# Performance work log

Measured on AMD Instinct MI355X. Metric: run time of the kernel, lower is better.

## Reference

```python
import jax, jax.numpy as jnp
import numpy as np

TAU = 2.0        # MultiStepLIFNode tau
ALPHA = 4.0      # sigmoid surrogate-gradient sharpness (spikingjelly default)
BN_EPS = 1e-5

@jax.custom_vjp
def heaviside(x):
    return (x >= 0.0).astype(x.dtype)

def _h_fwd(x):
    return (x >= 0.0).astype(x.dtype), x

def _h_bwd(res, g):
    s = jax.nn.sigmoid(ALPHA * res)
    return (g * ALPHA * s * (1.0 - s),)

heaviside.defvjp(_h_fwd, _h_bwd)

def lif(x_seq, v_threshold=1.0):
    """Multi-step LIF, hard reset to 0, decay_input, detach_reset. x_seq: [T, ...]"""
    def step(v, x):
        v = v + (x - v) / TAU
        spike = heaviside(v - v_threshold)
        v = v * (1.0 - jax.lax.stop_gradient(spike))
        return v, spike
    _, spikes = jax.lax.scan(step, jnp.zeros_like(x_seq[0]), x_seq)
    return spikes

def conv1x1_bn(x, w, gamma, beta, mean, var, bias=None):
    # x: [T,B,C,H,W]; 1x1 conv == channel matmul; BN in eval mode (affine fold)
    y = jnp.einsum('tbchw,oc->tbohw', x, w)
    if bias is not None:
        y = y + bias[None, None, :, None, None]
    inv = gamma / jnp.sqrt(var + BN_EPS)
    return y * inv[None, None, :, None, None] + (beta - mean * inv)[None, None, :, None, None]

def setup_inputs() -> dict:
    key = jax.random.key(0)
    T, B, C, H, W = 4, 16, 512, 32, 32
    ks = jax.random.split(key, 18)
    def w(k):
        return jax.random.normal(k, (C, C), jnp.float32) * (1.0 / np.sqrt(C))
    def vec_n(k):
        return jax.random.normal(k, (C,), jnp.float32) * 0.1
    def vec_p(k):
        return jax.random.uniform(k, (C,), jnp.float32, 0.5, 1.5)
    return {
        'x': jax.random.normal(ks[0], (T, B, C, H, W), jnp.float32),
        'q_w': w(ks[1]), 'q_gamma': vec_p(ks[2]), 'q_beta': vec_n(ks[3]),
        'q_mean': vec_n(ks[4]), 'q_var': vec_p(ks[5]),
        'k_w': w(ks[6]), 'k_gamma': vec_p(ks[7]), 'k_beta': vec_n(ks[8]),
        'k_mean': vec_n(ks[9]), 'k_var': vec_p(ks[10]),
        'proj_w': w(ks[11]), 'proj_b': vec_n(ks[12]), 'proj_gamma': vec_p(ks[13]),
        'proj_beta': vec_n(ks[14]), 'proj_mean': vec_n(ks[15]), 'proj_var': vec_p(ks[16]),
        'num_heads': 8,
    }

def reference(x, q_w, q_gamma, q_beta, q_mean, q_var,
              k_w, k_gamma, k_beta, k_mean, k_var,
              proj_w, proj_b, proj_gamma, proj_beta, proj_mean, proj_var,
              num_heads):
    T, B, C, H, W = x.shape
    hd = C // num_heads
    # Q / K branches: conv1x1 -> BN -> LIF spikes
    q = lif(conv1x1_bn(x, q_w, q_gamma, q_beta, q_mean, q_var))          # [T,B,C,H,W]
    k = lif(conv1x1_bn(x, k_w, k_gamma, k_beta, k_mean, k_var))          # [T,B,C,H,W]
    # sum over head-channel dim (keepdim), spike-gate at threshold 0.5
    q = q.reshape(T, B, num_heads, hd, H, W).sum(axis=3, keepdims=True)  # [T,B,nh,1,H,W]
    attn = lif(q, v_threshold=0.5)                                       # [T,B,nh,1,H,W]
    # elementwise gated attention (broadcast over head channels)
    y = (attn * k.reshape(T, B, num_heads, hd, H, W)).reshape(T, B, C, H, W)
    # projection: conv1x1(+bias) -> BN -> LIF
    y = lif(conv1x1_bn(y, proj_w, proj_gamma, proj_beta, proj_mean, proj_var, bias=proj_b))
    return y
```

## Files before the change

### kernel.cpp

```cpp
#include <hip/hip_runtime.h>
#include <cstdint>
#include <math.h>

#define TT 4
#define BB 16
#define CCH 512
#define HWD 1024
#define NHH 8
#define NW 16
#define MQK 1.5e-4
#define MPROJ 1.0e-4
#define CAPQ 49152
#define CAPP 16384
#define WTSZ 262144

typedef __attribute__((ext_vector_type(4))) float f32x4;
typedef __attribute__((ext_vector_type(8))) short s16x8;
typedef __attribute__((ext_vector_type(4))) uint32_t u32x4;

static __device__ __forceinline__ f32x4 MFMA(s16x8 a, s16x8 b, f32x4 c) {
    return __builtin_amdgcn_mfma_f32_16x16x32_bf16(a, b, c, 0, 0, 0);
}

static __device__ __forceinline__ uint32_t hi_pair(uint32_t u0, uint32_t u1) {
#if __has_builtin(__builtin_amdgcn_perm)
    return __builtin_amdgcn_perm(u1, u0, 0x07060302u);
#else
    return (u1 & 0xFFFF0000u) | (u0 >> 16);
#endif
}

struct SplitPair { uint32_t h, l; };

static __device__ __forceinline__ SplitPair split_pair(float f0, float f1) {
    const uint32_t u0 = __builtin_bit_cast(uint32_t, f0);
    const uint32_t u1 = __builtin_bit_cast(uint32_t, f1);
    SplitPair r;
    r.h = hi_pair(u0, u1);
    const float r0 = f0 - __builtin_bit_cast(float, u0 & 0xFFFF0000u);
    const float r1 = f1 - __builtin_bit_cast(float, u1 & 0xFFFF0000u);
    r.l = hi_pair(__builtin_bit_cast(uint32_t, r0), __builtin_bit_cast(uint32_t, r1));
    return r;
}

static __device__ __forceinline__ void load_split_frag(const float* p, s16x8& h, s16x8& l) {
    const float4 a = *(const float4*)p;
    const float4 b4 = *(const float4*)(p + 4);
    u32x4 hw_, lw_;
    const SplitPair p0 = split_pair(a.x, a.y);
    const SplitPair p1 = split_pair(a.z, a.w);
    const SplitPair p2 = split_pair(b4.x, b4.y);
    const SplitPair p3 = split_pair(b4.z, b4.w);
    hw_[0] = p0.h; lw_[0] = p0.l;
    hw_[1] = p1.h; lw_[1] = p1.l;
    hw_[2] = p2.h; lw_[2] = p2.l;
    hw_[3] = p3.h; lw_[3] = p3.l;
    h = __builtin_bit_cast(s16x8, hw_);
    l = __builtin_bit_cast(s16x8, lw_);
}

static __device__ __forceinline__ void glds16(const float* g, float* l) {
    __builtin_amdgcn_global_load_lds(
        (const __attribute__((address_space(1))) uint32_t*)g,
        (__attribute__((address_space(3))) uint32_t*)l, 16, 0, 0);
}

static __device__ __forceinline__ void probe_bf16(int lane, int rowD[4], int colD[4],
                                                  int& aRow, int& aKb, int& bCol, int& bKb)
{
    const f32x4 z = {0.f, 0.f, 0.f, 0.f};
    const short lv = (short)(__builtin_bit_cast(uint32_t, (float)lane) >> 16);
    const short one = (short)0x3F80;
    const s16x8 av = {lv, lv, lv, lv, lv, lv, lv, lv};
    const s16x8 ov = {one, one, one, one, one, one, one, one};
    const f32x4 pa = MFMA(av, ov, z);
    const f32x4 pb = MFMA(ov, av, z);
    bool A2 = false, B2 = false;
#pragma unroll
    for (int r = 0; r < 4; ++r) {
        const int va = (int)pa[r];
        if (((va - 48) & 127) == 0) { rowD[r] = (va - 48) >> 7; A2 = true; }
        else                        { rowD[r] = (va - 768) >> 5; }
        const int vb = (int)pb[r];
        if (((vb - 48) & 127) == 0) { colD[r] = (vb - 48) >> 7; B2 = true; }
        else                        { colD[r] = (vb - 768) >> 5; }
    }
    aRow = A2 ? (lane >> 2) : (lane & 15);
    aKb  = A2 ? (lane & 3) * 8 : (lane >> 4) * 8;
    bCol = B2 ? (lane >> 2) : (lane & 15);
    bKb  = B2 ? (lane & 3) * 8 : (lane >> 4) * 8;
}

__global__ void k_zero(unsigned int* ctr) {
    if (threadIdx.x < 2) ctr[threadIdx.x] = 0u;
}

__global__ __launch_bounds__(256) void k_prep(
    const float* __restrict__ qw, const float* __restrict__ kw, const float* __restrict__ pw,
    const float* __restrict__ qg, const float* __restrict__ qbe,
    const float* __restrict__ qm, const float* __restrict__ qva,
    const float* __restrict__ kg, const float* __restrict__ kbe,
    const float* __restrict__ km, const float* __restrict__ kva,
    const float* __restrict__ pg, const float* __restrict__ pbe,
    const float* __restrict__ pm, const float* __restrict__ pva,
    const float* __restrict__ pb,
    unsigned short* __restrict__ wt, double* __restrict__ bnc)
{
    const int bx = blockIdx.x;
    const int mat = bx >> 5, ot = bx & 31;
    const float* W = (mat == 0) ? qw : ((mat == 1) ? kw : pw);
    unsigned short* hi = wt + (size_t)(mat * 2 + 0) * WTSZ;
    unsigned short* lo = wt + (size_t)(mat * 2 + 1) * WTSZ;
#pragma unroll
    for (int it = 0; it < 4; ++it) {
        const int j = it * 256 + threadIdx.x;
        const int ks = j >> 6, sub = j & 63;
        const int kgrp = sub >> 4, row = sub & 15;
        const float* src = W + (size_t)(ot * 16 + row) * CCH + ks * 32 + kgrp * 8;
        s16x8 h, l;
        load_split_frag(src, h, l);
        *(s16x8*)&hi[((size_t)(ot * 16 + ks) * 64 + sub) * 8] = h;
        *(s16x8*)&lo[((size_t)(ot * 16 + ks) * 64 + sub) * 8] = l;
    }
    if (ot == 0) {
        const float* g  = (mat == 0) ? qg  : ((mat == 1) ? kg  : pg);
        const float* be = (mat == 0) ? qbe : ((mat == 1) ? kbe : pbe);
        const float* mn = (mat == 0) ? qm  : ((mat == 1) ? km  : pm);
        const float* va = (mat == 0) ? qva : ((mat == 1) ? kva : pva);
        for (int o = threadIdx.x; o < CCH; o += 256) {
            const double inv = (double)g[o] / sqrt((double)va[o] + 1e-5);
            double add = (double)be[o] - (double)mn[o] * inv;
            if (mat == 2) add = add + (double)pb[o] * inv;
            bnc[(size_t)(mat * CCH + o) * 2]     = inv;
            bnc[(size_t)(mat * CCH + o) * 2 + 1] = add;
        }
    }
}

__global__ __launch_bounds__(256, 4) void k_qk(
    const float* __restrict__ x,
    const unsigned short* __restrict__ wt, const double* __restrict__ bnc,
    uint32_t* __restrict__ qbits, uint32_t* __restrict__ kbits,
    unsigned int* __restrict__ ctr, uint32_t* __restrict__ list)
{
    __shared__ float Xs[2][4096];
    __shared__ uint32_t QB[2][2][TT][32];

    const int tid = threadIdx.x, lane = tid & 63, wid = tid >> 6;
    const int b   = blockIdx.z;
    const int o0  = blockIdx.y * 64, hw0 = blockIdx.x * 32;
    const int worow = (wid >> 1) * 32, whw = (wid & 1) * 16;

    int rowD[4], colD[4], aRow, aKb, bCol, bKb;
    probe_bf16(lane, rowD, colD, aRow, aKb, bCol, bKb);

    const int laneoff = ((aKb >> 3) * 16 + aRow) * 8;
    const int kgrp = bKb >> 3;
    const int roff = (whw + bCol) ^ ((kgrp & 1) << 4);
    const int otg0 = blockIdx.y * 4 + (wid >> 1) * 2;

    uint32_t gOff[4];
#pragma unroll
    for (int it = 0; it < 4; ++it) {
        const int ch = it * 256 + tid;
        const int t = ch >> 8, c = (ch >> 3) & 31, hw4p = ch & 7;
        const int ghw4 = hw4p ^ (((c >> 3) & 1) << 2);
        gOff[it] = (uint32_t)(((t * BB + b) * CCH + c) * HWD + hw0 + ghw4 * 4);
    }

    f32x4 aq[TT][2], ak[TT][2];
#pragma unroll
    for (int t = 0; t < TT; ++t)
#pragma unroll
        for (int ot = 0; ot < 2; ++ot) {
            aq[t][ot] = (f32x4){0.f, 0.f, 0.f, 0.f};
            ak[t][ot] = (f32x4){0.f, 0.f, 0.f, 0.f};
        }

    auto stage = [&](int ks, int buf) {
#pragma unroll
        for (int it = 0; it < 4; ++it)
            glds16(x + (size_t)gOff[it] + (size_t)ks * (32 * HWD),
                   &Xs[buf][(it * 256 + wid * 64) * 4]);
    };

    stage(0, 0);

    int cur = 0;
#pragma unroll 1
    for (int ks = 0; ks < 16; ++ks) {
        __syncthreads();
        if (ks < 15) stage(ks + 1, cur ^ 1);

        const size_t tb0 = ((size_t)(otg0 + 0) * 16 + ks) * 512 + laneoff;
        const size_t tb1 = ((size_t)(otg0 + 1) * 16 + ks) * 512 + laneoff;
        const s16x8 Aqh0 = *(const s16x8*)&wt[0 * WTSZ + tb0];
        const s16x8 Aql0 = *(const s16x8*)&wt[1 * WTSZ + tb0];
        const s16x8 Akh0 = *(const s16x8*)&wt[2 * WTSZ + tb0];
        const s16x8 Akl0 = *(const s16x8*)&wt[3 * WTSZ + tb0];
        const s16x8 Aqh1 = *(const s16x8*)&wt[0 * WTSZ + tb1];
        const s16x8 Aql1 = *(const s16x8*)&wt[1 * WTSZ + tb1];
        const s16x8 Akh1 = *(const s16x8*)&wt[2 * WTSZ + tb1];
        const s16x8 Akl1 = *(const s16x8*)&wt[3 * WTSZ + tb1];

        const float* Bb = Xs[cur];
#pragma unroll
        for (int t = 0; t < TT; ++t) {
            const float* Bp = Bb + (t * 32 + kgrp * 8) * 32 + roff;
            float w[8];
#pragma unroll
            for (int e = 0; e < 8; ++e) w[e] = Bp[e * 32];
            u32x4 bh, bl;
#pragma unroll
            for (int p = 0; p < 4; ++p) {
                const SplitPair sp = split_pair(w[2 * p], w[2 * p + 1]);
                bh[p] = sp.h; bl[p] = sp.l;
            }
            const s16x8 Bh = __builtin_bit_cast(s16x8, bh);
            const s16x8 Bl = __builtin_bit_cast(s16x8, bl);

            aq[t][0] = MFMA(Aqh0, Bh, aq[t][0]);
            aq[t][0] = MFMA(Aqh0, Bl, aq[t][0]);
            aq[t][0] = MFMA(Aql0, Bh, aq[t][0]);
            ak[t][0] = MFMA(Akh0, Bh, ak[t][0]);
            ak[t][0] = MFMA(Akh0, Bl, ak[t][0]);
            ak[t][0] = MFMA(Akl0, Bh, ak[t][0]);
            aq[t][1] = MFMA(Aqh1, Bh, aq[t][1]);
            aq[t][1] = MFMA(Aqh1, Bl, aq[t][1]);
            aq[t][1] = MFMA(Aql1, Bh, aq[t][1]);
            ak[t][1] = MFMA(Akh1, Bh, ak[t][1]);
            ak[t][1] = MFMA(Akh1, Bl, ak[t][1]);
            ak[t][1] = MFMA(Akl1, Bh, ak[t][1]);
        }
        cur ^= 1;
    }

    {
        int dum0, dum1, dum2, dum3;
        probe_bf16(lane, rowD, colD, dum0, dum1, dum2, dum3);
    }
    ((uint32_t*)QB)[tid] = 0u;
    ((uint32_t*)QB)[tid + 256] = 0u;
    __syncthreads();

    auto chains = [&](f32x4 (&acc)[TT][2], int br) {
#pragma unroll
        for (int ot = 0; ot < 2; ++ot)
#pragma unroll
            for (int r = 0; r < 4; ++r) {
                const int orow = worow + ot * 16 + rowD[r];
                const int o = o0 + orow;
                const double inv = bnc[(size_t)(br * CCH + o) * 2];
                const double add = bnc[(size_t)(br * CCH + o) * 2 + 1];
                const uint32_t bit = 1u << (orow & 31);
                const int ow = orow >> 5;
                const int hwq = whw + colD[r];
                double v = 0.0; bool fl = false;
#pragma unroll
                for (int t = 0; t < TT; ++t) {
                    const double y = (double)acc[t][ot][r] * inv + add;
                    v = v + (y - v) * 0.5;
                    if (fabs(v - 1.0) < MQK) fl = true;
                    if (v >= 1.0) { atomicOr(&QB[br][ow][t][hwq], bit); v = 0.0; }
                }
                if (fl) {
                    const unsigned int idx = atomicAdd(ctr, 1u);
                    if (idx < CAPQ)
                        list[idx] = (uint32_t)((br << 23) | (o << 14) | (b << 10) | (hw0 + hwq));
                }
            }
    };
    chains(aq, 0);
    chains(ak, 1);
    __syncthreads();

#pragma unroll
    for (int u = 0; u < 2; ++u) {
        const int idx = tid + u * 256;
        const int br = idx >> 8, ow = (idx >> 7) & 1, t = (idx >> 5) & 3, hwq = idx & 31;
        uint32_t* dst = br ? kbits : qbits;
        dst[((size_t)(t * BB + b) * NW + (o0 >> 5) + ow) * HWD + hw0 + hwq] = QB[br][ow][t][hwq];
    }
}

__global__ __launch_bounds__(256) void k_fix_qk(
    const float* __restrict__ x,
    const float* __restrict__ qw, const float* __restrict__ qg, const float* __restrict__ qbe,
    const float* __restrict__ qm, const float* __restrict__ qva,
    const float* __restrict__ kw, const float* __restrict__ kg, const float* __restrict__ kbe,
    const float* __restrict__ km, const float* __restrict__ kva,
    const unsigned int* __restrict__ ctr, const uint32_t* __restrict__ list,
    uint32_t* __restrict__ qbits, uint32_t* __restrict__ kbits)
{
    const int lane = threadIdx.x & 63;
    const int wg = (blockIdx.x * blockDim.x + threadIdx.x) >> 6;
    const int nw = (gridDim.x * blockDim.x) >> 6;
    unsigned int n = *ctr; if (n > CAPQ) n = CAPQ;

    for (unsigned int i = wg; i < n; i += nw) {
        const uint32_t e = list[i];
        const int br = (e >> 23) & 1, o = (e >> 14) & 511, b = (e >> 10) & 15, hw = e & 1023;
        const float* w = (br ? kw : qw) + (size_t)o * CCH;
        double dots[TT];
#pragma unroll
        for (int t = 0; t < TT; ++t) {
            double s = 0.0;
            for (int c = lane; c < CCH; c += 64)
                s += (double)w[c] * (double)x[((size_t)(t * BB + b) * CCH + c) * HWD + hw];
#pragma unroll
            for (int off = 32; off; off >>= 1) s += __shfl_xor(s, off);
            dots[t] = s;
        }
        if (lane == 0) {
            const float* g  = br ? kg  : qg;
            const float* be = br ? kbe : qbe;
            const float* mn = br ? km  : qm;
            const float* va = br ? kva : qva;
            const double inv = (double)g[o] / sqrt((double)va[o] + 1e-5);
            const double add = (double)be[o] - (double)mn[o] * inv;
            uint32_t* bits = br ? kbits : qbits;
            double v = 0.0;
#pragma unroll
            for (int t = 0; t < TT; ++t) {
                const double y = dots[t] * inv + add;
                v = v + (y - v) * 0.5;
                const size_t wa = ((size_t)(t * BB + b) * NW + (o >> 5)) * HWD + hw;
                const uint32_t bit = 1u << (o & 31);
                if (v >= 1.0) { atomicOr(&bits[wa], bit); v = 0.0; }
                else          { atomicAnd(&bits[wa], ~bit); }
            }
        }
    }
}

__global__ __launch_bounds__(256) void k_attn(
    const uint32_t* __restrict__ qbits, uint8_t* __restrict__ attn)
{
    const int idx = blockIdx.x * 256 + threadIdx.x;
    const int hw = idx & (HWD - 1);
    const int h  = (idx >> 10) & (NHH - 1);
    const int b  = idx >> 13;
    double v = 0.0;
#pragma unroll
    for (int t = 0; t < TT; ++t) {
        const uint32_t w0 = qbits[((size_t)(t * BB + b) * NW + h * 2    ) * HWD + hw];
        const uint32_t w1 = qbits[((size_t)(t * BB + b) * NW + h * 2 + 1) * HWD + hw];
        const double q = (double)(__popc(w0) + __popc(w1));
        v = v + (q - v) * 0.5;
        const uint8_t s = (v >= 0.5) ? (uint8_t)1 : (uint8_t)0;
        attn[((size_t)(t * BB + b) * NHH + h) * HWD + hw] = s;
        if (s) v = 0.0;
    }
}

__global__ __launch_bounds__(256, 3) void k_proj(
    const unsigned short* __restrict__ wt, const double* __restrict__ bnc,
    const uint32_t* __restrict__ kbits, const uint8_t* __restrict__ attn,
    float* __restrict__ out,
    unsigned int* __restrict__ ctr2, uint32_t* __restrict__ list2)
{
    __shared__ __align__(16) unsigned short Aw[2][2][8][512];

    const int tid = threadIdx.x, lane = tid & 63, wid = tid >> 6;
    const int b   = blockIdx.z;
    const int o0  = blockIdx.y * 128, hw0 = blockIdx.x * 32;
    const int worow = (wid >> 1) * 64, whw = (wid & 1) * 16;

    int rowD[4], colD[4], aRow, aKb, bCol, bKb;
    probe_bf16(lane, rowD, colD, aRow, aKb, bCol, bKb);
    const int laneoff = ((aKb >> 3) * 16 + aRow) * 8;
    const int hwB = hw0 + whw + bCol;
    const int otl0 = (wid >> 1) * 4;

    f32x4 acc[TT][4];
#pragma unroll
    for (int t = 0; t < TT; ++t)
#pragma unroll
        for (int ot = 0; ot < 4; ++ot) acc[t][ot] = (f32x4){0.f, 0.f, 0.f, 0.f};

    auto stageA = [&](int ks, int buf) {
#pragma unroll
        for (int i = 0; i < 4; ++i) {
            const int ch = wid * 4 + i;
            const int plane = ch >> 3, otl = ch & 7;
            const unsigned short* src = wt + (size_t)(4 + plane) * WTSZ
                + ((size_t)(blockIdx.y * 8 + otl) * 16 + ks) * 512 + (size_t)lane * 8;
            glds16((const float*)src, (float*)&Aw[buf][plane][otl][0]);
        }
    };

    uint32_t kvc[TT], avc[TT], kvn[TT], avn[TT];
    auto loadB = [&](int ks, uint32_t kv[TT], uint32_t av[TT]) {
#pragma unroll
        for (int t = 0; t < TT; ++t) {
            const size_t tb = (size_t)(t * BB + b);
            kv[t] = kbits[(tb * NW + ks) * HWD + hwB];
            av[t] = attn[(tb * NHH + (ks >> 1)) * HWD + hwB];
        }
    };

    stageA(0, 0);
    loadB(0, kvc, avc);
    __syncthreads();

    int cur = 0;
#pragma unroll 1
    for (int ks = 0; ks < 16; ++ks) {
        if (ks < 15) { stageA(ks + 1, cur ^ 1); loadB(ks + 1, kvn, avn); }

        s16x8 Ah[4], Al[4];
#pragma unroll
        for (int ot = 0; ot < 4; ++ot) {
            Ah[ot] = *(const s16x8*)&Aw[cur][0][otl0 + ot][laneoff];
            Al[ot] = *(const s16x8*)&Aw[cur][1][otl0 + ot][laneoff];
        }
#pragma unroll
        for (int t = 0; t < TT; ++t) {
            const uint32_t mask = avc[t] ? kvc[t] : 0u;
            const uint32_t byt = (mask >> bKb) & 0xFFu;
            u32x4 bw;
#pragma unroll
            for (int j = 0; j < 4; ++j)
                bw[j] = (((byt >> (2 * j)) & 1u) ? 0x3F80u : 0u)
                      | (((byt >> (2 * j + 1)) & 1u) ? 0x3F800000u : 0u);
            const s16x8 By = __builtin_bit_cast(s16x8, bw);
#pragma unroll
            for (int ot = 0; ot < 4; ++ot) {
                acc[t][ot] = MFMA(Ah[ot], By, acc[t][ot]);
                acc[t][ot] = MFMA(Al[ot], By, acc[t][ot]);
            }
        }

        if (ks < 15) {
#pragma unroll
            for (int t = 0; t < TT; ++t) { kvc[t] = kvn[t]; avc[t] = avn[t]; }
        }
        __syncthreads();
        cur ^= 1;
    }

#pragma unroll
    for (int ot = 0; ot < 4; ++ot)
#pragma unroll
        for (int r = 0; r < 4; ++r) {
            const int o = o0 + worow + ot * 16 + rowD[r];
            const int hwD = hw0 + whw + colD[r];
            const double inv = bnc[(size_t)(2 * CCH + o) * 2];
            const double add = bnc[(size_t)(2 * CCH + o) * 2 + 1];
            double v = 0.0; bool fl = false;
#pragma unroll
            for (int t = 0; t < TT; ++t) {
                const double y = (double)acc[t][ot][r] * inv + add;
                v = v + (y - v) * 0.5;
                if (fabs(v - 1.0) < MPROJ) fl = true;
                float s;
                if (v >= 1.0) { s = 1.0f; v = 0.0; } else { s = 0.0f; }
                out[((size_t)(t * BB + b) * CCH + o) * HWD + hwD] = s;
            }
            if (fl) {
                const unsigned int idx = atomicAdd(ctr2, 1u);
                if (idx < CAPP) list2[idx] = (uint32_t)((o << 14) | (b << 10) | hwD);
            }
        }
}

__global__ __launch_bounds__(256) void k_fix_proj(
    const float* __restrict__ pw, const float* __restrict__ pb,
    const float* __restrict__ pg, const float* __restrict__ pbe,
    const float* __restrict__ pm, const float* __restrict__ pva,
    const uint32_t* __restrict__ kbits, const uint8_t* __restrict__ attn,
    const unsigned int* __restrict__ ctr2, const uint32_t* __restrict__ list2,
    float* __restrict__ out)
{
    const int lane = threadIdx.x & 63;
    const int wg = (blockIdx.x * blockDim.x + threadIdx.x) >> 6;
    const int nw = (gridDim.x * blockDim.x) >> 6;
    unsigned int n = *ctr2; if (n > CAPP) n = CAPP;

    for (unsigned int i = wg; i < n; i += nw) {
        const uint32_t e = list2[i];
        const int o = (e >> 14) & 511, b = (e >> 10) & 15, hw = e & 1023;
        const float* w = pw + (size_t)o * CCH;
        double dots[TT];
#pragma unroll
        for (int t = 0; t < TT; ++t) {
            double s = 0.0;
            for (int c = lane; c < CCH; c += 64) {
                const uint32_t kv = kbits[((size_t)(t * BB + b) * NW + (c >> 5)) * HWD + hw];
                const uint32_t av = attn[((size_t)(t * BB + b) * NHH + (c >> 6)) * HWD + hw];
                if (av && ((kv >> (c & 31)) & 1u)) s += (double)w[c];
            }
#pragma unroll
            for (int off = 32; off; off >>= 1) s += __shfl_xor(s, off);
            dots[t] = s;
        }
        if (lane == 0) {
            const double inv = (double)pg[o] / sqrt((double)pva[o] + 1e-5);
            const double add = (double)pbe[o] - (double)pm[o] * inv;
            const double bias = (double)pb[o];
            double v = 0.0;
#pragma unroll
            for (int t = 0; t < TT; ++t) {
                const double y = (dots[t] + bias) * inv + add;
                v = v + (y - v) * 0.5;
                float s;
                if (v >= 1.0) { s = 1.0f; v = 0.0; } else { s = 0.0f; }
                out[((size_t)(t * BB + b) * CCH + o) * HWD + hw] = s;
            }
        }
    }
}

extern "C" void kernel_launch(void* const* d_in, const int* in_sizes, int n_in,
                              void* d_out, int out_size, void* d_ws, size_t ws_size,
                              hipStream_t stream)
{
    (void)in_sizes; (void)n_in; (void)out_size; (void)ws_size;

    const float* x   = (const float*)d_in[0];
    const float* qw  = (const float*)d_in[1];
    const float* qg  = (const float*)d_in[2];
    const float* qbe = (const float*)d_in[3];
    const float* qm  = (const float*)d_in[4];
    const float* qv  = (const float*)d_in[5];
    const float* kw  = (const float*)d_in[6];
    const float* kg  = (const float*)d_in[7];
    const float* kbe = (const float*)d_in[8];
    const float* km  = (const float*)d_in[9];
    const float* kv  = (const float*)d_in[10];
    const float* pw  = (const float*)d_in[11];
    const float* pb  = (const float*)d_in[12];
    const float* pg  = (const float*)d_in[13];
    const float* pbe = (const float*)d_in[14];
    const float* pm  = (const float*)d_in[15];
    const float* pv  = (const float*)d_in[16];

    uint8_t* base = (uint8_t*)d_ws;
    uint32_t* qbits = (uint32_t*)base;
    uint32_t* kbits = (uint32_t*)(base + 4194304);
    uint8_t*  attn  = base + 8388608;
    unsigned int* ctr = (unsigned int*)(base + 8912896);
    uint32_t* qklist  = (uint32_t*)(base + 8913152);
    uint32_t* prlist  = (uint32_t*)(base + 9109760);
    unsigned short* wtiles = (unsigned short*)(base + 9175296);
    double* bnc = (double*)(base + 12321024);
    float* out = (float*)d_out;

    k_zero<<<1, 64, 0, stream>>>(ctr);
    k_prep<<<96, 256, 0, stream>>>(qw, kw, pw, qg, qbe, qm, qv,
                                   kg, kbe, km, kv, pg, pbe, pm, pv, pb,
                                   wtiles, bnc);
    k_qk<<<dim3(HWD / 32, CCH / 64, BB), 256, 0, stream>>>(
        x, wtiles, bnc, qbits, kbits, ctr, qklist);
    k_fix_qk<<<256, 256, 0, stream>>>(x, qw, qg, qbe, qm, qv,
                                      kw, kg, kbe, km, kv, ctr, qklist, qbits, kbits);
    k_attn<<<(BB * NHH * HWD) / 256, 256, 0, stream>>>(qbits, attn);
    k_proj<<<dim3(HWD / 32, CCH / 128, BB), 256, 0, stream>>>(
        wtiles, bnc, kbits, attn, out, ctr + 1, prlist);
    k_fix_proj<<<64, 256, 0, stream>>>(pw, pb, pg, pbe, pm, pv,
                                       kbits, attn, ctr + 1, prlist, out);
}
```

Measured before the change: 392.3 us.

## Pre-split x into bf16 hi/lo channel-inner planes before the QK GEMM

Adds a k_xsplit pass that splits x into bf16 hi and lo parts once and transposes them into an hw-major, channel-inner layout in workspace. A new k_qk_pre kernel stages these planes straight into an XOR-swizzled LDS layout and reads MFMA B fragments with vector loads. This removes the per-fragment fp32 split work, which the old kernel repeated for every output-channel block. The cost is an extra full read and write of x, plus a large workspace requirement. If the workspace is too small, the old kernel is used instead.

After: 437.5 us. 1.12x slower.

```diff
diff --git a/kernel.cpp b/kernel.cpp
--- a/kernel.cpp
+++ b/kernel.cpp
@@ -13,6 +13,9 @@
 #define CAPQ 49152
 #define CAPP 16384
 #define WTSZ 262144
+#define XHOFF 12582912ULL
+#define XPLANE 33554432ULL
+#define WSNEED (XHOFF + 4ULL * XPLANE)
 
 typedef __attribute__((ext_vector_type(4))) float f32x4;
 typedef __attribute__((ext_vector_type(8))) short s16x8;
@@ -27,6 +30,13 @@
     return __builtin_amdgcn_perm(u1, u0, 0x07060302u);
 #else
     return (u1 & 0xFFFF0000u) | (u0 >> 16);
+#endif
+}
+static __device__ __forceinline__ uint32_t lo_pair(uint32_t u0, uint32_t u1) {
+#if __has_builtin(__builtin_amdgcn_perm)
+    return __builtin_amdgcn_perm(u1, u0, 0x05040100u);
+#else
+    return ((u1 & 0xFFFFu) << 16) | (u0 & 0xFFFFu);
 #endif
 }
 
@@ -41,6 +51,13 @@
     const float r1 = f1 - __builtin_bit_cast(float, u1 & 0xFFFF0000u);
     r.l = hi_pair(__builtin_bit_cast(uint32_t, r0), __builtin_bit_cast(uint32_t, r1));
     return r;
+}
+
+static __device__ __forceinline__ uint32_t packsplit(float f) {
+    const uint32_t u = __builtin_bit_cast(uint32_t, f);
+    const uint32_t hi = u & 0xFFFF0000u;
+    const float r = f - __builtin_bit_cast(float, hi);
+    return hi | (__builtin_bit_cast(uint32_t, r) >> 16);
 }
 
 static __device__ __forceinline__ void load_split_frag(const float* p, s16x8& h, s16x8& l) {
@@ -95,6 +112,43 @@
     if (threadIdx.x < 2) ctr[threadIdx.x] = 0u;
 }
 
+__global__ __launch_bounds__(256) void k_xsplit(
+    const float* __restrict__ x,
+    unsigned short* __restrict__ xh, unsigned short* __restrict__ xl)
+{
+    __shared__ uint32_t T[32][65];
+    const int tid = threadIdx.x;
+    const int tb = blockIdx.z;
+    const int c0 = blockIdx.y * 32, hw0 = blockIdx.x * 64;
+
+    {
+        const int c = tid >> 3, hwq = (tid & 7) * 8;
+        const float* src = &x[((size_t)tb * CCH + c0 + c) * HWD + hw0 + hwq];
+        const float4 a = *(const float4*)src;
+        const float4 b4 = *(const float4*)(src + 4);
+        T[c][hwq + 0] = packsplit(a.x);  T[c][hwq + 1] = packsplit(a.y);
+        T[c][hwq + 2] = packsplit(a.z);  T[c][hwq + 3] = packsplit(a.w);
+        T[c][hwq + 4] = packsplit(b4.x); T[c][hwq + 5] = packsplit(b4.y);
+        T[c][hwq + 6] = packsplit(b4.z); T[c][hwq + 7] = packsplit(b4.w);
+    }
+    __syncthreads();
+    {
+        const int hw = tid >> 2, cq = (tid & 3) * 8;
+        uint32_t v[8];
+#pragma unroll
+        for (int j = 0; j < 8; ++j) v[j] = T[cq + j][hw];
+        u32x4 h, l;
+#pragma unroll
+        for (int p = 0; p < 4; ++p) {
+            h[p] = hi_pair(v[2 * p], v[2 * p + 1]);
+            l[p] = lo_pair(v[2 * p], v[2 * p + 1]);
+        }
+        const size_t off = ((size_t)tb * HWD + hw0 + hw) * CCH + c0 + cq;
+        *(u32x4*)&xh[off] = h;
+        *(u32x4*)&xl[off] = l;
+    }
+}
+
 __global__ __launch_bounds__(256) void k_prep(
     const float* __restrict__ qw, const float* __restrict__ kw, const float* __restrict__ pw,
     const float* __restrict__ qg, const float* __restrict__ qbe,
@@ -137,13 +191,13 @@
     }
 }
 
-__global__ __launch_bounds__(256, 4) void k_qk(
-    const float* __restrict__ x,
+__global__ __launch_bounds__(256, 4) void k_qk_pre(
+    const unsigned short* __restrict__ xh, const unsigned short* __restrict__ xl,
     const unsigned short* __restrict__ wt, const double* __restrict__ bnc,
     uint32_t* __restrict__ qbits, uint32_t* __restrict__ kbits,
     unsigned int* __restrict__ ctr, uint32_t* __restrict__ list)
 {
-    __shared__ float Xs[2][4096];
+    __shared__ unsigned short XS[2][2][4096];
     __shared__ uint32_t QB[2][2][TT][32];
 
     const int tid = threadIdx.x, lane = tid & 63, wid = tid >> 6;
@@ -156,16 +210,18 @@
 
     const int laneoff = ((aKb >> 3) * 16 + aRow) * 8;
     const int kgrp = bKb >> 3;
-    const int roff = (whw + bCol) ^ ((kgrp & 1) << 4);
+    const int hwl  = whw + bCol;
+    const int physq = kgrp ^ ((hwl >> 1) & 3);
+    const int boff  = (hwl * 4 + physq) * 8;
     const int otg0 = blockIdx.y * 4 + (wid >> 1) * 2;
 
-    uint32_t gOff[4];
+    uint32_t gO[4];
 #pragma unroll
     for (int it = 0; it < 4; ++it) {
-        const int ch = it * 256 + tid;
-        const int t = ch >> 8, c = (ch >> 3) & 31, hw4p = ch & 7;
-        const int ghw4 = hw4p ^ (((c >> 3) & 1) << 2);
-        gOff[it] = (uint32_t)(((t * BB + b) * CCH + c) * HWD + hw0 + ghw4 * 4);
+        const int ch = (it & 1) * 256 + tid;
+        const int t = ch >> 7, hw = (ch >> 2) & 31, pq = ch & 3;
+        gO[it] = (uint32_t)(((size_t)(t * BB + b) * HWD + hw0 + hw) * CCH
+                            + (pq ^ ((hw >> 1) & 3)) * 8);
     }
 
     f32x4 aq[TT][2], ak[TT][2];
@@ -179,9 +235,11 @@
 
     auto stage = [&](int ks, int buf) {
 #pragma unroll
-        for (int it = 0; it < 4; ++it)
-            glds16(x + (size_t)gOff[it] + (size_t)ks * (32 * HWD),
-                   &Xs[buf][(it * 256 + wid * 64) * 4]);
+        for (int it = 0; it < 4; ++it) {
+            const unsigned short* sp = (it >> 1) ? xl : xh;
+            glds16((const float*)(sp + (size_t)gO[it] + ks * 32),
+                   (float*)&XS[buf][it >> 1][((it & 1) * 256 + wid * 64) * 8]);
+        }
     };
 
     stage(0, 0);
@@ -203,21 +261,11 @@
         const s16x8 Akh1 = *(const s16x8*)&wt[2 * WTSZ + tb1];
         const s16x8 Akl1 = *(const s16x8*)&wt[3 * WTSZ + tb1];
 
-        const float* Bb = Xs[cur];
 #pragma unroll
         for (int t = 0; t < TT; ++t) {
-            const float* Bp = Bb + (t * 32 + kgrp * 8) * 32 + roff;
-            float w[8];
-#pragma unroll
-            for (int e = 0; e < 8; ++e) w[e] = Bp[e * 32];
-            u32x4 bh, bl;
-#pragma unroll
-            for (int p = 0; p < 4; ++p) {
-                const SplitPair sp = split_pair(w[2 * p], w[2 * p + 1]);
-                bh[p] = sp.h; bl[p] = sp.l;
-            }
-            const s16x8 Bh = __builtin_bit_cast(s16x8, bh);
-            const s16x8 Bl = __builtin_bit_cast(s16x8, bl);
+            const int off = t * 1024 + boff;
+            const s16x8 Bh = *(const s16x8*)&XS[cur][0][off];
+            const s16x8 Bl = *(const s16x8*)&XS[cur][1][off];
 
             aq[t][0] = MFMA(Aqh0, Bh, aq[t][0]);
             aq[t][0] = MFMA(Aqh0, Bl, aq[t][0]);
@@ -235,10 +283,6 @@
         cur ^= 1;
     }
 
-    {
-        int dum0, dum1, dum2, dum3;
-        probe_bf16(lane, rowD, colD, dum0, dum1, dum2, dum3);
-    }
     ((uint32_t*)QB)[tid] = 0u;
     ((uint32_t*)QB)[tid + 256] = 0u;
     __syncthreads();
@@ -283,6 +327,152 @@
     }
 }
 
+__global__ __launch_bounds__(256, 4) void k_qk(
+    const float* __restrict__ x,
+    const unsigned short* __restrict__ wt, const double* __restrict__ bnc,
+    uint32_t* __restrict__ qbits, uint32_t* __restrict__ kbits,
+    unsigned int* __restrict__ ctr, uint32_t* __restrict__ list)
+{
+    __shared__ float Xs[2][4096];
+    __shared__ uint32_t QB[2][2][TT][32];
+
+    const int tid = threadIdx.x, lane = tid & 63, wid = tid >> 6;
+    const int b   = blockIdx.z;
+    const int o0  = blockIdx.y * 64, hw0 = blockIdx.x * 32;
+    const int worow = (wid >> 1) * 32, whw = (wid & 1) * 16;
+
+    int rowD[4], colD[4], aRow, aKb, bCol, bKb;
+    probe_bf16(lane, rowD, colD, aRow, aKb, bCol, bKb);
+
+    const int laneoff = ((aKb >> 3) * 16 + aRow) * 8;
+    const int kgrp = bKb >> 3;
+    const int roff = (whw + bCol) ^ ((kgrp & 1) << 4);
+    const int otg0 = blockIdx.y * 4 + (wid >> 1) * 2;
+
+    uint32_t gOff[4];
+#pragma unroll
+    for (int it = 0; it < 4; ++it) {
+        const int ch = it * 256 + tid;
+        const int t = ch >> 8, c = (ch >> 3) & 31, hw4p = ch & 7;
+        const int ghw4 = hw4p ^ (((c >> 3) & 1) << 2);
+        gOff[it] = (uint32_t)(((t * BB + b) * CCH + c) * HWD + hw0 + ghw4 * 4);
+    }
+
+    f32x4 aq[TT][2], ak[TT][2];
+#pragma unroll
+    for (int t = 0; t < TT; ++t)
+#pragma unroll
+        for (int ot = 0; ot < 2; ++ot) {
+            aq[t][ot] = (f32x4){0.f, 0.f, 0.f, 0.f};
+            ak[t][ot] = (f32x4){0.f, 0.f, 0.f, 0.f};
+        }
+
+    auto stage = [&](int ks, int buf) {
+#pragma unroll
+        for (int it = 0; it < 4; ++it)
+            glds16(x + (size_t)gOff[it] + (size_t)ks * (32 * HWD),
+                   &Xs[buf][(it * 256 + wid * 64) * 4]);
+    };
+
+    stage(0, 0);
+
+    int cur = 0;
+#pragma unroll 1
+    for (int ks = 0; ks < 16; ++ks) {
+        __syncthreads();
+        if (ks < 15) stage(ks + 1, cur ^ 1);
+
+        const size_t tb0 = ((size_t)(otg0 + 0) * 16 + ks) * 512 + laneoff;
+        const size_t tb1 = ((size_t)(otg0 + 1) * 16 + ks) * 512 + laneoff;
+        const s16x8 Aqh0 = *(const s16x8*)&wt[0 * WTSZ + tb0];
+        const s16x8 Aql0 = *(const s16x8*)&wt[1 * WTSZ + tb0];
+        const s16x8 Akh0 = *(const s16x8*)&wt[2 * WTSZ + tb0];
+        const s16x8 Akl0 = *(const s16x8*)&wt[3 * WTSZ + tb0];
+        const s16x8 Aqh1 = *(const s16x8*)&wt[0 * WTSZ + tb1];
+        const s16x8 Aql1 = *(const s16x8*)&wt[1 * WTSZ + tb1];
+        const s16x8 Akh1 = *(const s16x8*)&wt[2 * WTSZ + tb1];
+        const s16x8 Akl1 = *(const s16x8*)&wt[3 * WTSZ + tb1];
+
+        const float* Bb = Xs[cur];
+#pragma unroll
+        for (int t = 0; t < TT; ++t) {
+            const float* Bp = Bb + (t * 32 + kgrp * 8) * 32 + roff;
+            float w[8];
+#pragma unroll
+            for (int e = 0; e < 8; ++e) w[e] = Bp[e * 32];
+            u32x4 bh, bl;
+#pragma unroll
+            for (int p = 0; p < 4; ++p) {
+                const SplitPair sp = split_pair(w[2 * p], w[2 * p + 1]);
+                bh[p] = sp.h; bl[p] = sp.l;
+            }
+            const s16x8 Bh = __builtin_bit_cast(s16x8, bh);
+            const s16x8 Bl = __builtin_bit_cast(s16x8, bl);
+
+            aq[t][0] = MFMA(Aqh0, Bh, aq[t][0]);
+            aq[t][0] = MFMA(Aqh0, Bl, aq[t][0]);
+            aq[t][0] = MFMA(Aql0, Bh, aq[t][0]);
+            ak[t][0] = MFMA(Akh0, Bh, ak[t][0]);
+            ak[t][0] = MFMA(Akh0, Bl, ak[t][0]);
+            ak[t][0] = MFMA(Akl0, Bh, ak[t][0]);
+            aq[t][1] = MFMA(Aqh1, Bh, aq[t][1]);
+            aq[t][1] = MFMA(Aqh1, Bl, aq[t][1]);
+            aq[t][1] = MFMA(Aql1, Bh, aq[t][1]);
+            ak[t][1] = MFMA(Akh1, Bh, ak[t][1]);
+            ak[t][1] = MFMA(Akh1, Bl, ak[t][1]);
+            ak[t][1] = MFMA(Akl1, Bh, ak[t][1]);
+        }
+        cur ^= 1;
+    }
+
+    {
+        int dum0, dum1, dum2, dum3;
+        probe_bf16(lane, rowD, colD, dum0, dum1, dum2, dum3);
+    }
+    ((uint32_t*)QB)[tid] = 0u;
+    ((uint32_t*)QB)[tid + 256] = 0u;
+    __syncthreads();
+
+    auto chains = [&](f32x4 (&acc)[TT][2], int br) {
+#pragma unroll
+        for (int ot = 0; ot < 2; ++ot)
+#pragma unroll
+            for (int r = 0; r < 4; ++r) {
+                const int orow = worow + ot * 16 + rowD[r];
+                const int o = o0 + orow;
+                const double inv = bnc[(size_t)(br * CCH + o) * 2];
+                const double add = bnc[(size_t)(br * CCH + o) * 2 + 1];
+                const uint32_t bit = 1u << (orow & 31);
+                const int ow = orow >> 5;
+                const int hwq = whw + colD[r];
+                double v = 0.0; bool fl = false;
+#pragma unroll
+                for (int t = 0; t < TT; ++t) {
+                    const double y = (double)acc[t][ot][r] * inv + add;
+                    v = v + (y - v) * 0.5;
+                    if (fabs(v - 1.0) < MQK) fl = true;
+                    if (v >= 1.0) { atomicOr(&QB[br][ow][t][hwq], bit); v = 0.0; }
+                }
+                if (fl) {
+                    const unsigned int idx = atomicAdd(ctr, 1u);
+                    if (idx < CAPQ)
+                        list[idx] = (uint32_t)((br << 23) | (o << 14) | (b << 10) | (hw0 + hwq));
+                }
+            }
+    };
+    chains(aq, 0);
+    chains(ak, 1);
+    __syncthreads();
+
+#pragma unroll
+    for (int u = 0; u < 2; ++u) {
+        const int idx = tid + u * 256;
+        const int br = idx >> 8, ow = (idx >> 7) & 1, t = (idx >> 5) & 3, hwq = idx & 31;
+        uint32_t* dst = br ? kbits : qbits;
+        dst[((size_t)(t * BB + b) * NW + (o0 >> 5) + ow) * HWD + hw0 + hwq] = QB[br][ow][t][hwq];
+    }
+}
+
 __global__ __launch_bounds__(256) void k_fix_qk(
     const float* __restrict__ x,
     const float* __restrict__ qw, const float* __restrict__ qg, const float* __restrict__ qbe,
@@ -515,7 +705,7 @@
                               void* d_out, int out_size, void* d_ws, size_t ws_size,
                               hipStream_t stream)
 {
-    (void)in_sizes; (void)n_in; (void)out_size; (void)ws_size;
+    (void)in_sizes; (void)n_in; (void)out_size;
 
     const float* x   = (const float*)d_in[0];
     const float* qw  = (const float*)d_in[1];
@@ -544,14 +734,24 @@
     uint32_t* prlist  = (uint32_t*)(base + 9109760);
     unsigned short* wtiles = (unsigned short*)(base + 9175296);
     double* bnc = (double*)(base + 12321024);
+    unsigned short* xh = (unsigned short*)(base + XHOFF);
+    unsigned short* xl = xh + XPLANE;
     float* out = (float*)d_out;
+
+    const bool pre = ws_size >= WSNEED;
 
     k_zero<<<1, 64, 0, stream>>>(ctr);
     k_prep<<<96, 256, 0, stream>>>(qw, kw, pw, qg, qbe, qm, qv,
                                    kg, kbe, km, kv, pg, pbe, pm, pv, pb,
                                    wtiles, bnc);
-    k_qk<<<dim3(HWD / 32, CCH / 64, BB), 256, 0, stream>>>(
-        x, wtiles, bnc, qbits, kbits, ctr, qklist);
+    if (pre) {
+        k_xsplit<<<dim3(HWD / 64, CCH / 32, TT * BB), 256, 0, stream>>>(x, xh, xl);
+        k_qk_pre<<<dim3(HWD / 32, CCH / 64, BB), 256, 0, stream>>>(
+            xh, xl, wtiles, bnc, qbits, kbits, ctr, qklist);
+    } else {
+        k_qk<<<dim3(HWD / 32, CCH / 64, BB), 256, 0, stream>>>(
+            x, wtiles, bnc, qbits, kbits, ctr, qklist);
+    }
     k_fix_qk<<<256, 256, 0, stream>>>(x, qw, qg, qbe, qm, qv,
                                       kw, kg, kbe, km, kv, ctr, qklist, qbits, kbits);
     k_attn<<<(BB * NHH * HWD) / 256, 256, 0, stream>>>(qbits, attn);
```
